# Kernel optimization log

Measured on AMD Instinct MI355X. Metric: run time of the kernel, lower is better.

The kernel has to match this reference:

```python
import jax, jax.numpy as jnp
import numpy as np

KSIZE = 3
PAD = (KSIZE - 1) // 2
SIG = 0.3 * ((KSIZE - 1) * 0.5 - 1) + 0.8  # sigma_space == sigma_density == 0.8
INV2S2 = 1.0 / (2.0 * SIG * SIG)


def _gauss_space():
    c = KSIZE // 2
    xs = np.arange(KSIZE, dtype=np.float32)
    gx, gy = np.meshgrid(xs, xs, indexing='xy')
    w = np.exp(-(((gx - c) ** 2 + (gy - c) ** 2)) * INV2S2)
    w = w / w.sum()
    return jnp.asarray(w, dtype=jnp.float32)


def _patches(x):
    # x: [N,C,H,W] -> [N,C,H,W,k,k], zero padding (matches F.pad value=0)
    H, W = x.shape[-2], x.shape[-1]
    xp = jnp.pad(x, ((0, 0), (0, 0), (PAD, PAD), (PAD, PAD)))
    rows = []
    for i in range(KSIZE):
        cols = [xp[:, :, i:i + H, j:j + W] for j in range(KSIZE)]
        rows.append(jnp.stack(cols, axis=-1))
    return jnp.stack(rows, axis=-2)


def setup_inputs() -> dict:
    key = jax.random.key(0)
    k1, k2, k3 = jax.random.split(key, 3)
    B, V, C, H, W = 2, 4, 3, 512, 512
    depth = jax.random.uniform(k1, (B, V, 1, H, W), dtype=jnp.float32)
    color = jax.random.uniform(k2, (B, V, C, H, W), dtype=jnp.float32)
    mask = jax.random.uniform(k3, (B, V, 1, H, W), dtype=jnp.float32)
    return {"depth": depth, "color": color, "mask": mask}


def reference(depth, color, mask):
    B, V, C, H, W = color.shape
    d = depth.reshape(B * V, 1, H, W)
    m = mask.reshape(B * V, 1, H, W)
    c = color.reshape(B * V, C, H, W)

    dp = _patches(d)  # [N,1,H,W,k,k]
    cp = _patches(c)  # [N,C,H,W,k,k]
    mp = _patches(m)  # [N,1,H,W,k,k]

    # depth (density) gaussian weight, normalized per-pixel over the window
    wd = jnp.exp(-((dp - d[..., None, None]) ** 2) * INV2S2)
    wd = wd / wd.sum(axis=(-1, -2), keepdims=True)

    # color gaussian weight summed over channels, normalized per-pixel
    wc = jnp.exp(-((cp - c[..., None, None]) ** 2) * INV2S2).sum(axis=1, keepdims=True)
    wc = wc / wc.sum(axis=(-1, -2), keepdims=True)

    ws = _gauss_space().reshape(1, 1, 1, 1, KSIZE, KSIZE)

    w = wd * wc * ws * mp + 1e-7  # [N,1,H,W,k,k]
    out = (w * cp).sum(axis=(-1, -2)) / w.sum(axis=(-1, -2))  # [N,C,H,W]
    return out.reshape(B, V, C, H, W)
```

## Files before the change

kernel.cpp:

```cpp
#include <hip/hip_runtime.h>


typedef _Float16 h2 __attribute__((ext_vector_type(2)));

constexpr int HH = 512, WW = 512, HW = HH * WW;

__device__ __forceinline__ h2 H2c(float v) { return h2{(_Float16)v, (_Float16)v}; }
__device__ __forceinline__ h2 pkrtz(float a, float b) {
    return __builtin_bit_cast(h2, __builtin_amdgcn_cvt_pkrtz(a, b));
}

__device__ __forceinline__ h2 wpoly(h2 d) {
    h2 v = d * d + H2c(-0.5f);
    h2 w = H2c(-0.0537742f) + v * H2c(0.0105029f);
    w = H2c(0.206495f) + v * w;
    w = H2c(-0.528620f) + v * w;
    w = H2c(0.676634f) + v * w;
    return w;
}

#define WS0f 0.2724967f
#define WS1f 0.1247577f
#define WS2f 0.0571180f

struct RW  { h2 d[5], m[5], x[5], y[5], z[5]; };
struct Raw { float4 dm, mm, xm, ym, zm;
             float2 dl, dr, ml, mr, xl, xr, yl, yr, zl, zr; };
struct Acc { h2 swd, swc, st, s0, s1, s2; };

__global__ __launch_bounds__(256) void bilateral_v13(
    const float* __restrict__ depth,
    const float* __restrict__ color,
    const float* __restrict__ mask,
    float* __restrict__ out)
{
    const int lane = threadIdx.x & 63;
    const int wg   = blockIdx.x * 4 + (threadIdx.x >> 6);
    const int n    = wg >> 9;
    const int rem  = wg & 511;
    const int hp   = rem >> 1;
    const int half = rem & 1;
    const int rA   = hp * 2;
    const int c0   = half * 256 + lane * 4;

    const float* dptr = depth + (size_t)n * HW;
    const float* mptr = mask  + (size_t)n * HW;
    const float* xptr = color + (size_t)n * 3 * HW;
    const float* yptr = xptr + HW;
    const float* zptr = xptr + 2 * HW;

    const bool hasL = (c0 > 0);
    const bool hasR = (c0 < WW - 4);
    const int  colL = hasL ? c0 - 2 : c0;
    const int  colR = hasR ? c0 + 4 : c0;

#define LOADRAW(R_, r) do {                                                  \
    const int _o = (r) * WW;                                                 \
    R_.dm = *reinterpret_cast<const float4*>(dptr + _o + c0);                \
    R_.mm = *reinterpret_cast<const float4*>(mptr + _o + c0);                \
    R_.xm = *reinterpret_cast<const float4*>(xptr + _o + c0);                \
    R_.ym = *reinterpret_cast<const float4*>(yptr + _o + c0);                \
    R_.zm = *reinterpret_cast<const float4*>(zptr + _o + c0);                \
    R_.dl = *reinterpret_cast<const float2*>(dptr + _o + colL);              \
    R_.ml = *reinterpret_cast<const float2*>(mptr + _o + colL);              \
    R_.xl = *reinterpret_cast<const float2*>(xptr + _o + colL);              \
    R_.yl = *reinterpret_cast<const float2*>(yptr + _o + colL);              \
    R_.zl = *reinterpret_cast<const float2*>(zptr + _o + colL);              \
    R_.dr = *reinterpret_cast<const float2*>(dptr + _o + colR);              \
    R_.mr = *reinterpret_cast<const float2*>(mptr + _o + colR);              \
    R_.xr = *reinterpret_cast<const float2*>(xptr + _o + colR);              \
    R_.yr = *reinterpret_cast<const float2*>(yptr + _o + colR);              \
    R_.zr = *reinterpret_cast<const float2*>(zptr + _o + colR);              \
} while (0)

#define CVT1(dst, Qm, Ql, Qr) do {                                           \
    dst[0] = pkrtz(hasL ? (Ql).y : 0.0f, (Qm).x);                            \
    dst[1] = pkrtz((Qm).x, (Qm).y);                                          \
    dst[2] = pkrtz((Qm).y, (Qm).z);                                          \
    dst[3] = pkrtz((Qm).z, (Qm).w);                                          \
    dst[4] = pkrtz((Qm).w, hasR ? (Qr).x : 0.0f);                            \
} while (0)

#define CVTW(W_, R_) do {                                                    \
    CVT1(W_.d, R_.dm, R_.dl, R_.dr);                                         \
    CVT1(W_.m, R_.mm, R_.ml, R_.mr);                                         \
    CVT1(W_.x, R_.xm, R_.xl, R_.xr);                                         \
    CVT1(W_.y, R_.ym, R_.yl, R_.yr);                                         \
    CVT1(W_.z, R_.zm, R_.zl, R_.zr);                                         \
} while (0)

#define ZEROW(W_) do {                                                       \
    _Pragma("unroll") for (int _j = 0; _j < 5; ++_j) {                       \
        W_.d[_j] = h2{0,0}; W_.m[_j] = h2{0,0}; W_.x[_j] = h2{0,0};          \
        W_.y[_j] = h2{0,0}; W_.z[_j] = h2{0,0};                              \
    }                                                                        \
} while (0)

#define TAP(S_, pi, cD, cX, cY, cZ, WSC, A_) do {                            \
    const h2 _wd = wpoly(S_.d[pi] - (cD));                                   \
    const h2 _w0 = wpoly(S_.x[pi] - (cX));                                   \
    const h2 _w1 = wpoly(S_.y[pi] - (cY));                                   \
    const h2 _w2 = wpoly(S_.z[pi] - (cZ));                                   \
    const h2 _wc = _w0 + _w1 + _w2;                                          \
    const h2 _t  = (_wd * _wc) * (H2c(WSC) * S_.m[pi]);                      \
    A_.swd += _wd; A_.swc += _wc; A_.st += _t;                               \
    A_.s0 += _t * S_.x[pi]; A_.s1 += _t * S_.y[pi]; A_.s2 += _t * S_.z[pi];  \
} while (0)

#define ROWPASS_C(S_, A0_, A1_) do {                                         \
    TAP(S_, 0, S_.d[1], S_.x[1], S_.y[1], S_.z[1], WS1f, A0_);               \
    { const h2 _t = H2c(3.0f * WS0f) * S_.m[1];                              \
      A0_.swd += H2c(1.0f); A0_.swc += H2c(3.0f); A0_.st += _t;              \
      A0_.s0 += _t * S_.x[1]; A0_.s1 += _t * S_.y[1]; A0_.s2 += _t * S_.z[1]; } \
    TAP(S_, 2, S_.d[1], S_.x[1], S_.y[1], S_.z[1], WS1f, A0_);               \
    TAP(S_, 2, S_.d[3], S_.x[3], S_.y[3], S_.z[3], WS1f, A1_);               \
    { const h2 _t = H2c(3.0f * WS0f) * S_.m[3];                              \
      A1_.swd += H2c(1.0f); A1_.swc += H2c(3.0f); A1_.st += _t;              \
      A1_.s0 += _t * S_.x[3]; A1_.s1 += _t * S_.y[3]; A1_.s2 += _t * S_.z[3]; } \
    TAP(S_, 4, S_.d[3], S_.x[3], S_.y[3], S_.z[3], WS1f, A1_);               \
} while (0)

#define ROWPASS(S_, cd0,cx0,cy0,cz0, cd1,cx1,cy1,cz1, A0_, A1_, WSM, WSS) do { \
    TAP(S_, 0, cd0, cx0, cy0, cz0, WSS, A0_);                                \
    TAP(S_, 1, cd0, cx0, cy0, cz0, WSM, A0_);                                \
    TAP(S_, 2, cd0, cx0, cy0, cz0, WSS, A0_);                                \
    TAP(S_, 2, cd1, cx1, cy1, cz1, WSS, A1_);                                \
    TAP(S_, 3, cd1, cx1, cy1, cz1, WSM, A1_);                                \
    TAP(S_, 4, cd1, cx1, cy1, cz1, WSS, A1_);                                \
} while (0)

    const bool hasUp = (hp > 0);
    const bool hasDn = (hp < 255);
    const int  rUp = hasUp ? rA - 1 : rA;
    const int  rDn = hasDn ? rA + 2 : rA;

    Raw rawA, rawB;
    LOADRAW(rawA, rA);
    LOADRAW(rawB, rA + 1);

    RW A, B;
    CVTW(A, rawA);
    CVTW(B, rawB);

    Acc aa0{}, aa1{}, ab0{}, ab1{};

    ROWPASS_C(A, aa0, aa1);
    ROWPASS_C(B, ab0, ab1);

    Raw rawT;
    LOADRAW(rawT, rUp);

    ROWPASS(B, A.d[1],A.x[1],A.y[1],A.z[1], A.d[3],A.x[3],A.y[3],A.z[3],
            aa0, aa1, WS1f, WS2f);
    ROWPASS(A, B.d[1],B.x[1],B.y[1],B.z[1], B.d[3],B.x[3],B.y[3],B.z[3],
            ab0, ab1, WS1f, WS2f);

    const h2 cad0 = A.d[1], cad1 = A.d[3];
    const h2 cax0 = A.x[1], cax1 = A.x[3];
    const h2 cay0 = A.y[1], cay1 = A.y[3];
    const h2 caz0 = A.z[1], caz1 = A.z[3];
    const h2 cbd0 = B.d[1], cbd1 = B.d[3];
    const h2 cbx0 = B.x[1], cbx1 = B.x[3];
    const h2 cby0 = B.y[1], cby1 = B.y[3];
    const h2 cbz0 = B.z[1], cbz1 = B.z[3];

    RW T;
    if (hasUp) CVTW(T, rawT); else ZEROW(T);

    Raw rawT2;
    LOADRAW(rawT2, rDn);

    ROWPASS(T, cad0,cax0,cay0,caz0, cad1,cax1,cay1,caz1, aa0, aa1, WS1f, WS2f);

    if (hasDn) CVTW(T, rawT2); else ZEROW(T);
    ROWPASS(T, cbd0,cbx0,cby0,cbz0, cbd1,cbx1,cby1,cbz1, ab0, ab1, WS1f, WS2f);

#define EPI(A_, o0, o1, o2, i0, i1) do {                                     \
    {                                                                        \
        const float g   = (float)A_.st[0]                                    \
                        + 9e-7f * (float)A_.swd[0] * (float)A_.swc[0];       \
        const float inv = __builtin_amdgcn_rcpf(g);                          \
        o0[i0] = (float)A_.s0[0] * inv;                                      \
        o1[i0] = (float)A_.s1[0] * inv;                                      \
        o2[i0] = (float)A_.s2[0] * inv;                                      \
    }                                                                        \
    {                                                                        \
        const float g   = (float)A_.st[1]                                    \
                        + 9e-7f * (float)A_.swd[1] * (float)A_.swc[1];       \
        const float inv = __builtin_amdgcn_rcpf(g);                          \
        o0[i1] = (float)A_.s0[1] * inv;                                      \
        o1[i1] = (float)A_.s1[1] * inv;                                      \
        o2[i1] = (float)A_.s2[1] * inv;                                      \
    }                                                                        \
} while (0)

    float ra0[4], ra1[4], ra2[4], rb0[4], rb1[4], rb2[4];
    EPI(aa0, ra0, ra1, ra2, 0, 1);
    EPI(aa1, ra0, ra1, ra2, 2, 3);
    EPI(ab0, rb0, rb1, rb2, 0, 1);
    EPI(ab1, rb0, rb1, rb2, 2, 3);

    float* po = out + (size_t)n * 3 * HW + rA * WW + c0;
    *reinterpret_cast<float4*>(po)               = make_float4(ra0[0], ra0[1], ra0[2], ra0[3]);
    *reinterpret_cast<float4*>(po + HW)          = make_float4(ra1[0], ra1[1], ra1[2], ra1[3]);
    *reinterpret_cast<float4*>(po + 2 * HW)      = make_float4(ra2[0], ra2[1], ra2[2], ra2[3]);
    *reinterpret_cast<float4*>(po + WW)          = make_float4(rb0[0], rb0[1], rb0[2], rb0[3]);
    *reinterpret_cast<float4*>(po + WW + HW)     = make_float4(rb1[0], rb1[1], rb1[2], rb1[3]);
    *reinterpret_cast<float4*>(po + WW + 2 * HW) = make_float4(rb2[0], rb2[1], rb2[2], rb2[3]);
}

extern "C" void kernel_launch(void* const* d_in, const int* in_sizes, int n_in,
                              void* d_out, int out_size, void* d_ws, size_t ws_size,
                              hipStream_t stream) {
    const float* depth = (const float*)d_in[0];
    const float* color = (const float*)d_in[1];
    const float* mask  = (const float*)d_in[2];
    float* out = (float*)d_out;

    bilateral_v13<<<1024, 256, 0, stream>>>(depth, color, mask, out);
}
```

Before: 25.89 us.

## Process one output row per wave instead of two to raise parallelism

Each wave now computes a single output row (4 columns per lane) rather than a pair of rows, and the grid is doubled to 2048 blocks. This cuts per-thread register usage and doubles the number of waves, aiming for more occupancy and latency hiding. The cost is extra memory traffic: each input row is now loaded three times across neighbouring waves instead of roughly twice, mostly served from cache.

```diff
diff --git a/kernel.cpp b/kernel.cpp
--- a/kernel.cpp
+++ b/kernel.cpp
@@ -28,7 +28,7 @@
              float2 dl, dr, ml, mr, xl, xr, yl, yr, zl, zr; };
 struct Acc { h2 swd, swc, st, s0, s1, s2; };
 
-__global__ __launch_bounds__(256) void bilateral_v13(
+__global__ __launch_bounds__(256) void bilateral_v15(
     const float* __restrict__ depth,
     const float* __restrict__ color,
     const float* __restrict__ mask,
@@ -36,11 +36,10 @@
 {
     const int lane = threadIdx.x & 63;
     const int wg   = blockIdx.x * 4 + (threadIdx.x >> 6);
-    const int n    = wg >> 9;
-    const int rem  = wg & 511;
-    const int hp   = rem >> 1;
+    const int n    = wg >> 10;
+    const int rem  = wg & 1023;
+    const int r    = rem >> 1;
     const int half = rem & 1;
-    const int rA   = hp * 2;
     const int c0   = half * 256 + lane * 4;
 
     const float* dptr = depth + (size_t)n * HW;
@@ -54,8 +53,8 @@
     const int  colL = hasL ? c0 - 2 : c0;
     const int  colR = hasR ? c0 + 4 : c0;
 
-#define LOADRAW(R_, r) do {                                                  \
-    const int _o = (r) * WW;                                                 \
+#define LOADRAW(R_, rr) do {                                                 \
+    const int _o = (rr) * WW;                                                \
     R_.dm = *reinterpret_cast<const float4*>(dptr + _o + c0);                \
     R_.mm = *reinterpret_cast<const float4*>(mptr + _o + c0);                \
     R_.xm = *reinterpret_cast<const float4*>(xptr + _o + c0);                \
@@ -120,62 +119,45 @@
     TAP(S_, 4, S_.d[3], S_.x[3], S_.y[3], S_.z[3], WS1f, A1_);               \
 } while (0)
 
-#define ROWPASS(S_, cd0,cx0,cy0,cz0, cd1,cx1,cy1,cz1, A0_, A1_, WSM, WSS) do { \
-    TAP(S_, 0, cd0, cx0, cy0, cz0, WSS, A0_);                                \
-    TAP(S_, 1, cd0, cx0, cy0, cz0, WSM, A0_);                                \
-    TAP(S_, 2, cd0, cx0, cy0, cz0, WSS, A0_);                                \
-    TAP(S_, 2, cd1, cx1, cy1, cz1, WSS, A1_);                                \
-    TAP(S_, 3, cd1, cx1, cy1, cz1, WSM, A1_);                                \
-    TAP(S_, 4, cd1, cx1, cy1, cz1, WSS, A1_);                                \
+#define ROWPASS(S_, A0_, A1_) do {                                           \
+    TAP(S_, 0, cd0, cx0, cy0, cz0, WS2f, A0_);                               \
+    TAP(S_, 1, cd0, cx0, cy0, cz0, WS1f, A0_);                               \
+    TAP(S_, 2, cd0, cx0, cy0, cz0, WS2f, A0_);                               \
+    TAP(S_, 2, cd1, cx1, cy1, cz1, WS2f, A1_);                               \
+    TAP(S_, 3, cd1, cx1, cy1, cz1, WS1f, A1_);                               \
+    TAP(S_, 4, cd1, cx1, cy1, cz1, WS2f, A1_);                               \
 } while (0)
 
-    const bool hasUp = (hp > 0);
-    const bool hasDn = (hp < 255);
-    const int  rUp = hasUp ? rA - 1 : rA;
-    const int  rDn = hasDn ? rA + 2 : rA;
+    const bool hasUp = (r > 0);
+    const bool hasDn = (r < HH - 1);
 
-    Raw rawA, rawB;
-    LOADRAW(rawA, rA);
-    LOADRAW(rawB, rA + 1);
+    Raw rawT, rawC;
+    LOADRAW(rawT, hasUp ? r - 1 : r);
+    LOADRAW(rawC, r);
 
-    RW A, B;
-    CVTW(A, rawA);
-    CVTW(B, rawB);
+    Acc a0{}, a1{};
 
-    Acc aa0{}, aa1{}, ab0{}, ab1{};
-
-    ROWPASS_C(A, aa0, aa1);
-    ROWPASS_C(B, ab0, ab1);
-
-    Raw rawT;
-    LOADRAW(rawT, rUp);
-
-    ROWPASS(B, A.d[1],A.x[1],A.y[1],A.z[1], A.d[3],A.x[3],A.y[3],A.z[3],
-            aa0, aa1, WS1f, WS2f);
-    ROWPASS(A, B.d[1],B.x[1],B.y[1],B.z[1], B.d[3],B.x[3],B.y[3],B.z[3],
-            ab0, ab1, WS1f, WS2f);
-
-    const h2 cad0 = A.d[1], cad1 = A.d[3];
-    const h2 cax0 = A.x[1], cax1 = A.x[3];
-    const h2 cay0 = A.y[1], cay1 = A.y[3];
-    const h2 caz0 = A.z[1], caz1 = A.z[3];
-    const h2 cbd0 = B.d[1], cbd1 = B.d[3];
-    const h2 cbx0 = B.x[1], cbx1 = B.x[3];
-    const h2 cby0 = B.y[1], cby1 = B.y[3];
-    const h2 cbz0 = B.z[1], cbz1 = B.z[3];
+    RW C;
+    CVTW(C, rawC);
+    const h2 cd0 = C.d[1], cd1 = C.d[3];
+    const h2 cx0 = C.x[1], cx1 = C.x[3];
+    const h2 cy0 = C.y[1], cy1 = C.y[3];
+    const h2 cz0 = C.z[1], cz1 = C.z[3];
+    ROWPASS_C(C, a0, a1);
 
     RW T;
     if (hasUp) CVTW(T, rawT); else ZEROW(T);
 
-    Raw rawT2;
-    LOADRAW(rawT2, rDn);
+    Raw rawN;
+    LOADRAW(rawN, hasDn ? r + 1 : r);
 
-    ROWPASS(T, cad0,cax0,cay0,caz0, cad1,cax1,cay1,caz1, aa0, aa1, WS1f, WS2f);
+    ROWPASS(T, a0, a1);
 
-    if (hasDn) CVTW(T, rawT2); else ZEROW(T);
-    ROWPASS(T, cbd0,cbx0,cby0,cbz0, cbd1,cbx1,cby1,cbz1, ab0, ab1, WS1f, WS2f);
+    if (hasDn) CVTW(T, rawN); else ZEROW(T);
+    ROWPASS(T, a0, a1);
 
-#define EPI(A_, o0, o1, o2, i0, i1) do {                                     \
+    float o0[4], o1[4], o2[4];
+#define EPI(A_, i0, i1) do {                                                 \
     {                                                                        \
         const float g   = (float)A_.st[0]                                    \
                         + 9e-7f * (float)A_.swd[0] * (float)A_.swc[0];       \
@@ -194,19 +176,13 @@
     }                                                                        \
 } while (0)
 
-    float ra0[4], ra1[4], ra2[4], rb0[4], rb1[4], rb2[4];
-    EPI(aa0, ra0, ra1, ra2, 0, 1);
-    EPI(aa1, ra0, ra1, ra2, 2, 3);
-    EPI(ab0, rb0, rb1, rb2, 0, 1);
-    EPI(ab1, rb0, rb1, rb2, 2, 3);
+    EPI(a0, 0, 1);
+    EPI(a1, 2, 3);
 
-    float* po = out + (size_t)n * 3 * HW + rA * WW + c0;
-    *reinterpret_cast<float4*>(po)               = make_float4(ra0[0], ra0[1], ra0[2], ra0[3]);
-    *reinterpret_cast<float4*>(po + HW)          = make_float4(ra1[0], ra1[1], ra1[2], ra1[3]);
-    *reinterpret_cast<float4*>(po + 2 * HW)      = make_float4(ra2[0], ra2[1], ra2[2], ra2[3]);
-    *reinterpret_cast<float4*>(po + WW)          = make_float4(rb0[0], rb0[1], rb0[2], rb0[3]);
-    *reinterpret_cast<float4*>(po + WW + HW)     = make_float4(rb1[0], rb1[1], rb1[2], rb1[3]);
-    *reinterpret_cast<float4*>(po + WW + 2 * HW) = make_float4(rb2[0], rb2[1], rb2[2], rb2[3]);
+    float* po = out + (size_t)n * 3 * HW + r * WW + c0;
+    *reinterpret_cast<float4*>(po)          = make_float4(o0[0], o0[1], o0[2], o0[3]);
+    *reinterpret_cast<float4*>(po + HW)     = make_float4(o1[0], o1[1], o1[2], o1[3]);
+    *reinterpret_cast<float4*>(po + 2 * HW) = make_float4(o2[0], o2[1], o2[2], o2[3]);
 }
 
 extern "C" void kernel_launch(void* const* d_in, const int* in_sizes, int n_in,
@@ -217,5 +193,5 @@
     const float* mask  = (const float*)d_in[2];
     float* out = (float*)d_out;
 
-    bilateral_v13<<<1024, 256, 0, stream>>>(depth, color, mask, out);
+    bilateral_v15<<<2048, 256, 0, stream>>>(depth, color, mask, out);
 }
```

New measurement: 28.17 us. +8.8%, slower.
